# Kernel optimization log

Hardware: AMD Instinct MI355X
Metric: run time of the kernel (lower is better)

The kernel has to match this reference:

```python
import jax, jax.numpy as jnp
import numpy as np

N_EMBD = 384
HEAD_SIZE = 64
B, T = 16, 2048


def setup_inputs() -> dict:
    key = jax.random.key(0)
    ks = jax.random.split(key, 7)
    s = 1.0 / np.sqrt(N_EMBD)
    return {
        "x": jax.random.normal(ks[0], (B, T, N_EMBD), dtype=jnp.float32),
        "Wq": jax.random.uniform(ks[1], (N_EMBD, HEAD_SIZE), jnp.float32, -s, s),
        "bq": jax.random.uniform(ks[2], (HEAD_SIZE,), jnp.float32, -s, s),
        "Wk": jax.random.uniform(ks[3], (N_EMBD, HEAD_SIZE), jnp.float32, -s, s),
        "bk": jax.random.uniform(ks[4], (HEAD_SIZE,), jnp.float32, -s, s),
        "Wv": jax.random.uniform(ks[5], (N_EMBD, HEAD_SIZE), jnp.float32, -s, s),
        "bv": jax.random.uniform(ks[6], (HEAD_SIZE,), jnp.float32, -s, s),
    }


def reference(x, Wq, bq, Wk, bk, Wv, bv):
    # QKV projections: [B,T,C] @ [C,H] -> [B,T,H]
    q = x @ Wq + bq
    k = x @ Wk + bk
    v = x @ Wv + bv
    scale = k.shape[-1] ** (-0.5)
    # NOTE: original forward applies NO causal mask (tril buffer unused).
    scores = jnp.einsum("bqh,bkh->bqk", q, k) * scale  # [B,T,T]
    wmap = jax.nn.softmax(scores, axis=-1)
    # dropout is identity in eval mode
    out = jnp.einsum("bqk,bkh->bqh", wmap, v)  # [B,T,H]
    return out
```

## Files before the change

kernel.cpp:

```cpp
#include <hip/hip_runtime.h>
#include <hip/hip_bf16.h>
#include <cstdint>

typedef unsigned short u16;
typedef __attribute__((ext_vector_type(8))) short short8;
typedef __attribute__((ext_vector_type(4))) short short4v;
typedef __attribute__((ext_vector_type(4))) float f32x4;

#define MFMA16(a, b, c) __builtin_amdgcn_mfma_f32_16x16x32_bf16((a), (b), (c), 0, 0, 0)

constexpr int Bn   = 16;
constexpr int Tn   = 2048;
constexpr int Cn   = 384;
constexpr int Hn   = 64;
constexpr long NTOK = (long)Bn * Tn;
constexpr long NELT = NTOK * Hn;
constexpr int SPLITS = 3;

#define QSCALE 0.18033688011112042f

__device__ __forceinline__ u16 f2bf(float f) {
  union { float f; uint32_t u; } c; c.f = f;
  uint32_t u = c.u;
  return (u16)((u + 0x7fffu + ((u >> 16) & 1u)) >> 16);
}

__device__ __forceinline__ uint32_t pkbf(float a, float b) {
  uint32_t d;
  asm("v_cvt_pk_bf16_f32 %0, %1, %2" : "=v"(d) : "v"(a), "v"(b));
  return d;
}

__device__ __forceinline__ short8 ldx8(const float* p) {
  const float4 f0 = *reinterpret_cast<const float4*>(p);
  const float4 f1 = *reinterpret_cast<const float4*>(p + 4);
  union { short8 s8; uint32_t u[4]; } r;
  r.u[0] = pkbf(f0.x, f0.y); r.u[1] = pkbf(f0.z, f0.w);
  r.u[2] = pkbf(f1.x, f1.y); r.u[3] = pkbf(f1.z, f1.w);
  return r.s8;
}

__device__ __forceinline__ void gl16(const u16* g, const u16* l) {
  __builtin_amdgcn_global_load_lds(
      (const __attribute__((address_space(1))) void*)g,
      (__attribute__((address_space(3))) void*)l, 16, 0, 0);
}

__global__ __launch_bounds__(256) void wtrans(
    const float* __restrict__ Wq, const float* __restrict__ Wk,
    const float* __restrict__ Wv, u16* __restrict__ wtd)
{
  __shared__ u16 tile[64][65];
  const int m  = blockIdx.x / 6;
  const int kc = blockIdx.x % 6;
  const float* W = (m == 0) ? Wq : (m == 1) ? Wk : Wv;
  const int t = threadIdx.x;

  {
    const int kr = t >> 2, seg = t & 3;
    const float* src = W + (size_t)(kc * 64 + kr) * Hn + seg * 16;
    #pragma unroll
    for (int j = 0; j < 4; ++j) {
      const float4 f = *reinterpret_cast<const float4*>(src + j * 4);
      u16* p = &tile[kr][seg * 16 + j * 4];
      p[0] = f2bf(f.x); p[1] = f2bf(f.y); p[2] = f2bf(f.z); p[3] = f2bf(f.w);
    }
  }
  __syncthreads();
  {
    const int hr = t >> 2, seg = t & 3;
    union { short8 s; u16 u[8]; } o0, o1;
    #pragma unroll
    for (int j = 0; j < 8; ++j) o0.u[j] = tile[seg * 16 + j][hr];
    #pragma unroll
    for (int j = 0; j < 8; ++j) o1.u[j] = tile[seg * 16 + 8 + j][hr];
    u16* dst = wtd + ((size_t)m * 64 + hr) * Cn + kc * 64 + seg * 16;
    *reinterpret_cast<short8*>(dst)     = o0.s;
    *reinterpret_cast<short8*>(dst + 8) = o1.s;
  }
}

__global__ __launch_bounds__(256, 2) void qkv_proj(
    const float* __restrict__ x, const u16* __restrict__ wtd,
    const float* __restrict__ bq, const float* __restrict__ bk,
    const float* __restrict__ bv,
    u16* __restrict__ oq, u16* __restrict__ ok, u16* __restrict__ ovt)
{
  __shared__ u16 wbuf[3][3 * 64 * 64];

  const int t    = threadIdx.x;
  const int lane = t & 63;
  const int w    = t >> 6;
  const int l15  = lane & 15;
  const int lh   = lane >> 4;
  const long r0  = (long)blockIdx.x * 64;

  int srcoff[6];
  #pragma unroll
  for (int i = 0; i < 6; ++i) {
    const int g = i * 256 + t;
    const int r = g >> 3, c = g & 7;
    srcoff[i] = r * Cn + ((c ^ (r & 7)) << 3);
  }
  const int ldsb = w * 64 * 8;

  const float* xrow = x + (r0 + w * 16 + l15) * Cn;

  const int cks0 = ((lh)     ^ (l15 & 7)) << 3;
  const int cks1 = ((lh + 4) ^ (l15 & 7)) << 3;

  f32x4 acc[3][4];
  #pragma unroll
  for (int m = 0; m < 3; ++m)
    #pragma unroll
    for (int n = 0; n < 4; ++n) acc[m][n] = f32x4{0.f, 0.f, 0.f, 0.f};

  #pragma unroll
  for (int i = 0; i < 6; ++i)
    gl16(wtd + srcoff[i], &wbuf[0][(i * 256) * 8 + ldsb]);
  short8 aCur0 = ldx8(xrow + lh * 8);
  short8 aCur1 = ldx8(xrow + 32 + lh * 8);
  #pragma unroll
  for (int i = 0; i < 6; ++i)
    gl16(wtd + 64 + srcoff[i], &wbuf[1][(i * 256) * 8 + ldsb]);
  short8 aNx10 = ldx8(xrow + 64 + lh * 8);
  short8 aNx11 = ldx8(xrow + 96 + lh * 8);
  short8 aNx20, aNx21;
  asm volatile("s_waitcnt vmcnt(14)" ::: "memory");
  __builtin_amdgcn_s_barrier();
  __builtin_amdgcn_sched_barrier(0);

  for (int kc = 0; kc < 6; ++kc) {
    const int cb = kc % 3;
    const int sb = (kc + 2) % 3;
    if (kc + 2 < 6) {
      #pragma unroll
      for (int i = 0; i < 6; ++i)
        gl16(wtd + (kc + 2) * 64 + srcoff[i], &wbuf[sb][(i * 256) * 8 + ldsb]);
      const float* p = xrow + (kc + 2) * 64 + lh * 8;
      aNx20 = ldx8(p);
      aNx21 = ldx8(p + 32);
    }

    const u16* wc = &wbuf[cb][0];
    #pragma unroll
    for (int m = 0; m < 3; ++m)
      #pragma unroll
      for (int n = 0; n < 4; ++n) {
        const int row = m * 64 + n * 16 + l15;
        const short8 b0 = *reinterpret_cast<const short8*>(&wc[row * 64 + cks0]);
        acc[m][n] = MFMA16(aCur0, b0, acc[m][n]);
        const short8 b1 = *reinterpret_cast<const short8*>(&wc[row * 64 + cks1]);
        acc[m][n] = MFMA16(aCur1, b1, acc[m][n]);
      }

    if (kc + 1 < 6) {
      if (kc + 2 < 6) asm volatile("s_waitcnt vmcnt(14)" ::: "memory");
      else            asm volatile("s_waitcnt vmcnt(4)"  ::: "memory");
      __builtin_amdgcn_s_barrier();
      __builtin_amdgcn_sched_barrier(0);
      aCur0 = aNx10; aCur1 = aNx11;
      aNx10 = aNx20; aNx11 = aNx21;
    }
  }

  {
    const float* bias[2] = {bq, bk};
    u16*         dst[2]  = {oq, ok};
    const float  scl[2]  = {QSCALE, 1.0f};
    #pragma unroll
    for (int m = 0; m < 2; ++m) {
      #pragma unroll
      for (int n = 0; n < 4; ++n) {
        int col = n * 16 + l15;
        float bb = bias[m][col];
        #pragma unroll
        for (int r = 0; r < 4; ++r) {
          int row = lh * 4 + r;
          dst[m][(r0 + w * 16 + row) * Hn + col] = f2bf((acc[m][n][r] + bb) * scl[m]);
        }
      }
    }
  }
  {
    const long g    = r0 + w * 16 + lh * 4;
    const long bidx = g >> 11;
    const long tloc = g & 2047;
    const int  u    = (int)(tloc & 63);
    const long tb   = tloc & ~63L;
    const int  slotb = 32 * ((u >> 5) & 1) + 8 * ((u >> 2) & 3) + 4 * ((u >> 4) & 1);
    #pragma unroll
    for (int n = 0; n < 4; ++n) {
      int col = n * 16 + l15;
      float bb = bv[col];
      short4v pk;
      #pragma unroll
      for (int r = 0; r < 4; ++r) pk[r] = (short)f2bf(acc[2][n][r] + bb);
      *reinterpret_cast<short4v*>(ovt + (bidx * Hn + col) * Tn + tb + slotb) = pk;
    }
  }
}

__global__ __launch_bounds__(256, 3) void flash_attn(
    const u16* __restrict__ q, const u16* __restrict__ k,
    const u16* __restrict__ vt, u16* __restrict__ opart,
    float* __restrict__ lpart)
{
  __shared__ u16 kbuf[3][64 * 64];
  __shared__ u16 vbuf[3][64 * 64];

  const int t    = threadIdx.x;
  const int lane = t & 63;
  const int w    = t >> 6;
  const int l15  = lane & 15;
  const int lh   = lane >> 4;
  const int swz_id = (blockIdx.x & 7) * 96 + (blockIdx.x >> 3);
  const int b     = swz_id / 48;
  const int rsw   = swz_id % 48;
  const int split = rsw / 16;
  const int qt    = rsw % 16;
  const long rowbase = (long)b * Tn + qt * 128;
  const int it0 = (split * 32) / 3;
  const int it1 = ((split + 1) * 32) / 3;

  short8 aq[2][2];
  #pragma unroll
  for (int qg = 0; qg < 2; ++qg) {
    const u16* qrow = q + (rowbase + w * 32 + qg * 16 + l15) * Hn;
    aq[qg][0] = *reinterpret_cast<const short8*>(qrow + lh * 8);
    aq[qg][1] = *reinterpret_cast<const short8*>(qrow + 32 + lh * 8);
  }

  union { short8 s8; uint32_t u[4]; } ON;
  #pragma unroll
  for (int i = 0; i < 4; ++i) ON.u[i] = 0x3F803F80u;

  f32x4 o[2][4];
  #pragma unroll
  for (int qg = 0; qg < 2; ++qg)
    #pragma unroll
    for (int m = 0; m < 4; ++m) o[qg][m] = f32x4{0.f, 0.f, 0.f, 0.f};
  f32x4 ls0 = f32x4{0.f, 0.f, 0.f, 0.f};
  f32x4 ls1 = f32x4{0.f, 0.f, 0.f, 0.f};

  const u16* kb_g = k  + (long)b * Tn * Hn;
  const u16* vb_g = vt + (long)b * Hn * Tn;

  const int g0 = t, g1 = 256 + t;
  const int r0g = g0 >> 3, c0g = g0 & 7;
  const int r1g = g1 >> 3, c1g = g1 & 7;
  const long ksrc0 = (long)r0g * Hn + ((c0g ^ (r0g & 7)) << 3);
  const long ksrc1 = (long)r1g * Hn + ((c1g ^ (r1g & 7)) << 3);
  const long vsrc0 = (long)r0g * Tn + ((c0g ^ (r0g & 7)) << 3);
  const long vsrc1 = (long)r1g * Tn + ((c1g ^ (r1g & 7)) << 3);
  const int wb0 = w * 64 * 8;
  const int wb1 = wb0 + 256 * 8;

  const int swz  = l15 & 7;
  const int cks0 = ((0 * 4 + lh) ^ swz) << 3;
  const int cks1 = ((1 * 4 + lh) ^ swz) << 3;
  const int rfr  = l15 * 64;

  {
    const u16* kt = kb_g + (long)it0 * 64 * Hn;
    const u16* vp = vb_g + it0 * 64;
    gl16(kt + ksrc0, &kbuf[0][wb0]);
    gl16(kt + ksrc1, &kbuf[0][wb1]);
    gl16(vp + vsrc0, &vbuf[0][wb0]);
    gl16(vp + vsrc1, &vbuf[0][wb1]);
    const u16* kt1 = kb_g + (long)(it0 + 1) * 64 * Hn;
    const u16* vp1 = vb_g + (it0 + 1) * 64;
    gl16(kt1 + ksrc0, &kbuf[1][wb0]);
    gl16(kt1 + ksrc1, &kbuf[1][wb1]);
    gl16(vp1 + vsrc0, &vbuf[1][wb0]);
    gl16(vp1 + vsrc1, &vbuf[1][wb1]);
  }
  asm volatile("s_waitcnt vmcnt(4)" ::: "memory");
  __builtin_amdgcn_s_barrier();
  __builtin_amdgcn_sched_barrier(0);

  for (int it = it0; it < it1; ++it) {
    const int cb = (it - it0) % 3;
    const int sb = (it - it0 + 2) % 3;
    if (it + 2 < it1) {
      const u16* kt = kb_g + (long)(it + 2) * 64 * Hn;
      const u16* vp = vb_g + (it + 2) * 64;
      gl16(kt + ksrc0, &kbuf[sb][wb0]);
      gl16(kt + ksrc1, &kbuf[sb][wb1]);
      gl16(vp + vsrc0, &vbuf[sb][wb0]);
      gl16(vp + vsrc1, &vbuf[sb][wb1]);
    }

    const u16* kc  = &kbuf[cb][0];
    const u16* vcb = &vbuf[cb][0];

    f32x4 s0[4], s1[4];
    #pragma unroll
    for (int n = 0; n < 4; ++n) { s0[n] = f32x4{0.f,0.f,0.f,0.f}; s1[n] = f32x4{0.f,0.f,0.f,0.f}; }
    __builtin_amdgcn_s_setprio(1);
    #pragma unroll
    for (int n = 0; n < 4; ++n) {
      const short8 ak0 = *reinterpret_cast<const short8*>(&kc[n * 1024 + rfr + cks0]);
      const short8 ak1 = *reinterpret_cast<const short8*>(&kc[n * 1024 + rfr + cks1]);
      s0[n] = MFMA16(ak0, aq[0][0], s0[n]);
      s0[n] = MFMA16(ak1, aq[0][1], s0[n]);
      s1[n] = MFMA16(ak0, aq[1][0], s1[n]);
      s1[n] = MFMA16(ak1, aq[1][1], s1[n]);
    }
    __builtin_amdgcn_s_setprio(0);

    #pragma unroll
    for (int n = 0; n < 4; ++n)
      #pragma unroll
      for (int r = 0; r < 4; ++r) {
        s0[n][r] = __builtin_amdgcn_exp2f(s0[n][r]);
        s1[n][r] = __builtin_amdgcn_exp2f(s1[n][r]);
      }

    union { short8 s8; uint32_t u[4]; } B00, B01, B10, B11;
    B00.u[0] = pkbf(s0[0][0], s0[0][1]); B00.u[1] = pkbf(s0[0][2], s0[0][3]);
    B00.u[2] = pkbf(s0[1][0], s0[1][1]); B00.u[3] = pkbf(s0[1][2], s0[1][3]);
    B01.u[0] = pkbf(s0[2][0], s0[2][1]); B01.u[1] = pkbf(s0[2][2], s0[2][3]);
    B01.u[2] = pkbf(s0[3][0], s0[3][1]); B01.u[3] = pkbf(s0[3][2], s0[3][3]);
    B10.u[0] = pkbf(s1[0][0], s1[0][1]); B10.u[1] = pkbf(s1[0][2], s1[0][3]);
    B10.u[2] = pkbf(s1[1][0], s1[1][1]); B10.u[3] = pkbf(s1[1][2], s1[1][3]);
    B11.u[0] = pkbf(s1[2][0], s1[2][1]); B11.u[1] = pkbf(s1[2][2], s1[2][3]);
    B11.u[2] = pkbf(s1[3][0], s1[3][1]); B11.u[3] = pkbf(s1[3][2], s1[3][3]);

    __builtin_amdgcn_s_setprio(1);
    #pragma unroll
    for (int m = 0; m < 4; ++m) {
      const short8 av0 = *reinterpret_cast<const short8*>(&vcb[m * 1024 + rfr + cks0]);
      const short8 av1 = *reinterpret_cast<const short8*>(&vcb[m * 1024 + rfr + cks1]);
      o[0][m] = MFMA16(av0, B00.s8, o[0][m]);
      o[0][m] = MFMA16(av1, B01.s8, o[0][m]);
      o[1][m] = MFMA16(av0, B10.s8, o[1][m]);
      o[1][m] = MFMA16(av1, B11.s8, o[1][m]);
    }
    ls0 = MFMA16(ON.s8, B00.s8, ls0);
    ls0 = MFMA16(ON.s8, B01.s8, ls0);
    ls1 = MFMA16(ON.s8, B10.s8, ls1);
    ls1 = MFMA16(ON.s8, B11.s8, ls1);
    __builtin_amdgcn_s_setprio(0);

    if (it + 1 < it1) {
      if (it + 2 < it1) asm volatile("s_waitcnt vmcnt(4)" ::: "memory");
      else              asm volatile("s_waitcnt vmcnt(0)" ::: "memory");
      __builtin_amdgcn_s_barrier();
      __builtin_amdgcn_sched_barrier(0);
    }
  }

  #pragma unroll
  for (int qg = 0; qg < 2; ++qg) {
    const float tot = (qg == 0) ? ls0[0] : ls1[0];
    const long qrow = rowbase + w * 32 + qg * 16 + l15;
    u16* od = opart + ((long)split * NELT) + qrow * Hn;
    #pragma unroll
    for (int m = 0; m < 4; ++m) {
      uint32_t p0 = pkbf(o[qg][m][0], o[qg][m][1]);
      uint32_t p1 = pkbf(o[qg][m][2], o[qg][m][3]);
      uint32_t* dst = reinterpret_cast<uint32_t*>(od + m * 16 + lh * 4);
      dst[0] = p0; dst[1] = p1;
    }
    if (lh == 0) lpart[(long)split * NTOK + qrow] = tot;
  }
}

__global__ __launch_bounds__(256) void combine(
    const u16* __restrict__ op, const float* __restrict__ lp,
    float* __restrict__ out)
{
  const long idx  = (long)blockIdx.x * 256 + threadIdx.x;
  const long base = idx * 8;
  const long row  = base >> 6;
  float lsum = lp[row] + lp[NTOK + row] + lp[2 * NTOK + row];
  const float linv = 1.0f / lsum;

  float acc[8] = {0.f, 0.f, 0.f, 0.f, 0.f, 0.f, 0.f, 0.f};
  #pragma unroll
  for (int s = 0; s < SPLITS; ++s) {
    union { short8 v; u16 u[8]; } pk;
    pk.v = *reinterpret_cast<const short8*>(op + s * NELT + base);
    #pragma unroll
    for (int j = 0; j < 8; ++j) {
      union { uint32_t u; float f; } c; c.u = ((uint32_t)pk.u[j]) << 16;
      acc[j] += c.f;
    }
  }
  float4 r0, r1;
  r0.x = acc[0] * linv; r0.y = acc[1] * linv; r0.z = acc[2] * linv; r0.w = acc[3] * linv;
  r1.x = acc[4] * linv; r1.y = acc[5] * linv; r1.z = acc[6] * linv; r1.w = acc[7] * linv;
  *reinterpret_cast<float4*>(out + base)     = r0;
  *reinterpret_cast<float4*>(out + base + 4) = r1;
}

extern "C" void kernel_launch(void* const* d_in, const int* in_sizes, int n_in,
                              void* d_out, int out_size, void* d_ws, size_t ws_size,
                              hipStream_t stream) {
  const float* x  = (const float*)d_in[0];
  const float* Wq = (const float*)d_in[1];
  const float* bq = (const float*)d_in[2];
  const float* Wk = (const float*)d_in[3];
  const float* bk = (const float*)d_in[4];
  const float* Wv = (const float*)d_in[5];
  const float* bv = (const float*)d_in[6];
  float* out = (float*)d_out;

  u16* qs  = (u16*)d_ws;
  u16* ks  = qs + NELT;
  u16* vs  = ks + NELT;
  u16* wtd = vs + NELT;
  u16* op  = wtd + 3 * 64 * Cn;
  float* lp = (float*)(op + (long)SPLITS * NELT);

  hipLaunchKernelGGL(wtrans, dim3(18), dim3(256), 0, stream, Wq, Wk, Wv, wtd);
  hipLaunchKernelGGL(qkv_proj, dim3((int)(NTOK / 64)), dim3(256), 0, stream,
                     x, wtd, bq, bk, bv, qs, ks, vs);
  hipLaunchKernelGGL(flash_attn, dim3(16 * 16 * SPLITS), dim3(256), 0, stream,
                     qs, ks, vs, op, lp);
  hipLaunchKernelGGL(combine, dim3((int)(NELT / 8 / 256)), dim3(256), 0, stream,
                     op, lp, out);
}
```

Before: 52.78 us.

## Use four KV splits with a paired four-buffer LDS prefetch schedule

After: 52.26 us. Within noise of the previous version (-1.0%).

```diff
diff --git a/kernel.cpp b/kernel.cpp
--- a/kernel.cpp
+++ b/kernel.cpp
@@ -15,7 +15,7 @@
 constexpr int Hn   = 64;
 constexpr long NTOK = (long)Bn * Tn;
 constexpr long NELT = NTOK * Hn;
-constexpr int SPLITS = 3;
+constexpr int SPLITS = 4;
 
 #define QSCALE 0.18033688011112042f
 
@@ -201,27 +201,26 @@
   }
 }
 
-__global__ __launch_bounds__(256, 3) void flash_attn(
+__global__ __launch_bounds__(256, 2) void flash_attn(
     const u16* __restrict__ q, const u16* __restrict__ k,
     const u16* __restrict__ vt, u16* __restrict__ opart,
     float* __restrict__ lpart)
 {
-  __shared__ u16 kbuf[3][64 * 64];
-  __shared__ u16 vbuf[3][64 * 64];
+  __shared__ u16 kbuf[4][64 * 64];
+  __shared__ u16 vbuf[4][64 * 64];
 
   const int t    = threadIdx.x;
   const int lane = t & 63;
   const int w    = t >> 6;
   const int l15  = lane & 15;
   const int lh   = lane >> 4;
-  const int swz_id = (blockIdx.x & 7) * 96 + (blockIdx.x >> 3);
-  const int b     = swz_id / 48;
-  const int rsw   = swz_id % 48;
-  const int split = rsw / 16;
-  const int qt    = rsw % 16;
+  const int swz_id = (blockIdx.x & 7) * 128 + (blockIdx.x >> 3);
+  const int b     = swz_id / 64;
+  const int rem   = swz_id % 64;
+  const int split = rem / 16;
+  const int qt    = rem % 16;
   const long rowbase = (long)b * Tn + qt * 128;
-  const int it0 = (split * 32) / 3;
-  const int it1 = ((split + 1) * 32) / 3;
+  const int it0 = split * 8;
 
   short8 aq[2][2];
   #pragma unroll
@@ -261,38 +260,18 @@
   const int cks1 = ((1 * 4 + lh) ^ swz) << 3;
   const int rfr  = l15 * 64;
 
-  {
-    const u16* kt = kb_g + (long)it0 * 64 * Hn;
-    const u16* vp = vb_g + it0 * 64;
-    gl16(kt + ksrc0, &kbuf[0][wb0]);
-    gl16(kt + ksrc1, &kbuf[0][wb1]);
-    gl16(vp + vsrc0, &vbuf[0][wb0]);
-    gl16(vp + vsrc1, &vbuf[0][wb1]);
-    const u16* kt1 = kb_g + (long)(it0 + 1) * 64 * Hn;
-    const u16* vp1 = vb_g + (it0 + 1) * 64;
-    gl16(kt1 + ksrc0, &kbuf[1][wb0]);
-    gl16(kt1 + ksrc1, &kbuf[1][wb1]);
-    gl16(vp1 + vsrc0, &vbuf[1][wb0]);
-    gl16(vp1 + vsrc1, &vbuf[1][wb1]);
-  }
-  asm volatile("s_waitcnt vmcnt(4)" ::: "memory");
-  __builtin_amdgcn_s_barrier();
-  __builtin_amdgcn_sched_barrier(0);
-
-  for (int it = it0; it < it1; ++it) {
-    const int cb = (it - it0) % 3;
-    const int sb = (it - it0 + 2) % 3;
-    if (it + 2 < it1) {
-      const u16* kt = kb_g + (long)(it + 2) * 64 * Hn;
-      const u16* vp = vb_g + (it + 2) * 64;
-      gl16(kt + ksrc0, &kbuf[sb][wb0]);
-      gl16(kt + ksrc1, &kbuf[sb][wb1]);
-      gl16(vp + vsrc0, &vbuf[sb][wb0]);
-      gl16(vp + vsrc1, &vbuf[sb][wb1]);
-    }
-
-    const u16* kc  = &kbuf[cb][0];
-    const u16* vcb = &vbuf[cb][0];
+  auto stage = [&](int it, int bs) {
+    const u16* kt = kb_g + (long)it * 64 * Hn;
+    const u16* vp = vb_g + it * 64;
+    gl16(kt + ksrc0, &kbuf[bs][wb0]);
+    gl16(kt + ksrc1, &kbuf[bs][wb1]);
+    gl16(vp + vsrc0, &vbuf[bs][wb0]);
+    gl16(vp + vsrc1, &vbuf[bs][wb1]);
+  };
+
+  auto tile_compute = [&](int bs) {
+    const u16* kc  = &kbuf[bs][0];
+    const u16* vcb = &vbuf[bs][0];
 
     f32x4 s0[4], s1[4];
     #pragma unroll
@@ -342,12 +321,31 @@
     ls1 = MFMA16(ON.s8, B10.s8, ls1);
     ls1 = MFMA16(ON.s8, B11.s8, ls1);
     __builtin_amdgcn_s_setprio(0);
-
-    if (it + 1 < it1) {
-      if (it + 2 < it1) asm volatile("s_waitcnt vmcnt(4)" ::: "memory");
-      else              asm volatile("s_waitcnt vmcnt(0)" ::: "memory");
+  };
+
+  stage(it0 + 0, 0);
+  stage(it0 + 1, 1);
+  stage(it0 + 2, 2);
+  stage(it0 + 3, 3);
+  asm volatile("s_waitcnt vmcnt(8)" ::: "memory");
+  __builtin_amdgcn_s_barrier();
+  __builtin_amdgcn_sched_barrier(0);
+
+  #pragma unroll
+  for (int p = 0; p < 4; ++p) {
+    const int bA = (2 * p) & 3;
+    const int bB = (2 * p + 1) & 3;
+    tile_compute(bA);
+    tile_compute(bB);
+
+    if (p < 3) {
+      asm volatile("s_waitcnt vmcnt(0)" ::: "memory");
       __builtin_amdgcn_s_barrier();
       __builtin_amdgcn_sched_barrier(0);
+      if (p < 2) {
+        stage(it0 + 2 * p + 4, bA);
+        stage(it0 + 2 * p + 5, bB);
+      }
     }
   }
 
@@ -374,7 +372,9 @@
   const long idx  = (long)blockIdx.x * 256 + threadIdx.x;
   const long base = idx * 8;
   const long row  = base >> 6;
-  float lsum = lp[row] + lp[NTOK + row] + lp[2 * NTOK + row];
+  float lsum = 0.f;
+  #pragma unroll
+  for (int s = 0; s < SPLITS; ++s) lsum += lp[s * NTOK + row];
   const float linv = 1.0f / lsum;
 
   float acc[8] = {0.f, 0.f, 0.f, 0.f, 0.f, 0.f, 0.f, 0.f};
```
